# Kernel optimization log

Measured on AMD Instinct MI355X. Metric: run time of the kernel, lower is better.

Reference implementation:

```python
import jax, jax.numpy as jnp
import numpy as np

B, V, E = 8, 12288, 98304   # batch, nodes (healpix nside=32), edges (~8 nbrs/node)
FIN, FOUT, K = 256, 256, 4  # channels, Chebyshev order
EPS = 1e-5                  # BatchNorm1d eps


def setup_inputs() -> dict:
    key = jax.random.key(0)
    ks = jax.random.split(key, 5)
    x = jax.random.normal(ks[0], (B, V, FIN), jnp.float32)
    edge_src = jax.random.randint(ks[1], (E,), 0, V, dtype=jnp.int32)
    edge_dst = jax.random.randint(ks[2], (E,), 0, V, dtype=jnp.int32)
    edge_weight = jax.random.normal(ks[3], (E,), jnp.float32) * 0.3
    scale = (2.0 / (FIN * K)) ** 0.5  # kaiming-style init over K*Fin fan-in
    weight = jax.random.normal(ks[4], (K, FIN, FOUT), jnp.float32) * scale
    bias = jnp.zeros((FOUT,), jnp.float32)
    gamma = jnp.ones((FOUT,), jnp.float32)
    beta = jnp.zeros((FOUT,), jnp.float32)
    return {"x": x, "edge_weight": edge_weight, "weight": weight, "bias": bias,
            "gamma": gamma, "beta": beta, "edge_src": edge_src, "edge_dst": edge_dst}


def reference(x, edge_weight, weight, bias, gamma, beta, edge_src, edge_dst):
    # --- ConvCheb: Chebyshev polynomial recursion over sparse Laplacian ---
    xt = x.transpose(1, 0, 2)  # [V, B, Fin] (node-major for segment scatter)

    def lmul(y):  # sparse L @ y, y: [V, B, Fin]
        msg = edge_weight[:, None, None] * y[edge_src]          # [E, B, Fin]
        return jax.ops.segment_sum(msg, edge_dst, num_segments=V)

    xs = [xt]                                  # T_0(L) x = x
    if K > 1:
        xs.append(lmul(xt))                    # T_1(L) x = L x
    for _ in range(2, K):
        xs.append(2.0 * lmul(xs[-1]) - xs[-2])  # T_k = 2 L T_{k-1} - T_{k-2}
    xk = jnp.stack(xs)                         # [K, V, B, Fin]

    out = jnp.einsum('kvbi,kio->bvo', xk, weight) + bias  # [B, V, Fout]

    # --- BatchNorm1d over channels (training-mode batch stats over B,V) ---
    mean = out.mean(axis=(0, 1))
    var = out.var(axis=(0, 1))  # biased variance, as torch uses for normalization
    out = gamma * (out - mean) * jax.lax.rsqrt(var + EPS) + beta

    return jax.nn.relu(out)
```

## Files before the change

kernel.cpp:

```cpp
#include <hip/hip_runtime.h>

#define Vn    12288
#define En    98304
#define Mrows 98304

typedef unsigned short u16;
typedef u16   u16x8  __attribute__((ext_vector_type(8)));
typedef __bf16 bf16x8 __attribute__((ext_vector_type(8)));
typedef float f32x4  __attribute__((ext_vector_type(4)));

__device__ __forceinline__ float bf2f(u16 u) {
    union { float f; unsigned int i; } c; c.i = ((unsigned int)u) << 16; return c.f;
}
__device__ __forceinline__ u16 f2bf(float f) {
    union { float f; unsigned int i; } c; c.f = f;
    unsigned int r = c.i + 0x7fffu + ((c.i >> 16) & 1u);
    return (u16)(r >> 16);
}
__device__ __forceinline__ void load_lds16(const void* g, void* l) {
    __builtin_amdgcn_global_load_lds(
        (const __attribute__((address_space(1))) void*)g,
        (__attribute__((address_space(3))) void*)l, 16, 0, 0);
}

__global__ void cvt_k(const float* __restrict__ x, u16* __restrict__ xb) {
    int v = blockIdx.x;
    int t = threadIdx.x;
    int b = t >> 5, i = (t & 31) * 8;
    const float* p = x + ((size_t)b * Vn + v) * 256 + i;
    f32x4 a0 = *(const f32x4*)p;
    f32x4 a1 = *(const f32x4*)(p + 4);
    u16x8 r;
    #pragma unroll
    for (int j = 0; j < 4; ++j) { r[j] = f2bf(a0[j]); r[4 + j] = f2bf(a1[j]); }
    *(u16x8*)(xb + (size_t)v * 2048 + b * 256 + i) = r;
}

__global__ void wtrans_k(const float* __restrict__ w, u16* __restrict__ wt) {
    int kk = blockIdx.x;
    int o  = threadIdx.x;
    wt[(size_t)o * 1024 + kk] = f2bf(w[(size_t)kk * 256 + o]);
}

__global__ void count_k(const int* __restrict__ dst, int* __restrict__ counts) {
    int e = blockIdx.x * 256 + threadIdx.x;
    atomicAdd(&counts[dst[e]], 1);
}

__global__ void scan_k(const int* __restrict__ counts, int* __restrict__ row_start,
                       int* __restrict__ cursor) {
    __shared__ int par[1024];
    int t = threadIdx.x;
    int base = t * 12;
    int s = 0;
    #pragma unroll
    for (int i = 0; i < 12; ++i) s += counts[base + i];
    par[t] = s;
    __syncthreads();
    for (int off = 1; off < 1024; off <<= 1) {
        int v_ = (t >= off) ? par[t - off] : 0;
        __syncthreads();
        par[t] += v_;
        __syncthreads();
    }
    int run = (t == 0) ? 0 : par[t - 1];
    for (int i = 0; i < 12; ++i) {
        row_start[base + i] = run;
        cursor[base + i]    = run;
        run += counts[base + i];
    }
    if (t == 1023) row_start[Vn] = En;
}

__global__ void fill_k(const int* __restrict__ src, const int* __restrict__ dst,
                       const float* __restrict__ ew, int* __restrict__ cursor,
                       int* __restrict__ csr_src, float* __restrict__ csr_w) {
    int e = blockIdx.x * 256 + threadIdx.x;
    int d = dst[e];
    int p = atomicAdd(&cursor[d], 1);
    csr_src[p] = src[e];
    csr_w[p]   = ew[e];
}

template<int PREV>
__global__ __launch_bounds__(256)
void lmul_k(const u16* __restrict__ yb, const u16* __restrict__ prevb,
            u16* __restrict__ outb, const int* __restrict__ row_start,
            const int* __restrict__ csr_src, const float* __restrict__ csr_w)
{
    __shared__ int   s_s[256];
    __shared__ float s_w[256];
    int slice = blockIdx.x & 7;
    int v0    = (blockIdx.x >> 3) * 8;
    int tid   = threadIdx.x;
    int s0    = row_start[v0];
    int tot   = row_start[v0 + 8] - s0;
    if (tid < tot && tid < 256) {
        s_s[tid] = csr_src[s0 + tid];
        s_w[tid] = csr_w[s0 + tid];
    }
    __syncthreads();
    int g = tid >> 5, t = tid & 31;
    int v = v0 + g;
    int base = row_start[v] - s0;
    int cnt  = row_start[v + 1] - row_start[v];
    size_t soff = (size_t)slice * 256 + (size_t)t * 8;
    float acc[8] = {0.f,0.f,0.f,0.f,0.f,0.f,0.f,0.f};
    for (int j = 0; j < cnt; ++j) {
        int s; float w;
        if (base + j < 256) { s = s_s[base + j]; w = s_w[base + j]; }
        else { s = csr_src[s0 + base + j]; w = csr_w[s0 + base + j]; }
        u16x8 u = *(const u16x8*)(yb + (size_t)s * 2048 + soff);
        #pragma unroll
        for (int j8 = 0; j8 < 8; ++j8) acc[j8] += w * bf2f(u[j8]);
    }
    u16x8 r;
    if (PREV) {
        u16x8 pu = *(const u16x8*)(prevb + (size_t)v * 2048 + soff);
        #pragma unroll
        for (int j8 = 0; j8 < 8; ++j8) r[j8] = f2bf(2.0f * acc[j8] - bf2f(pu[j8]));
    } else {
        #pragma unroll
        for (int j8 = 0; j8 < 8; ++j8) r[j8] = f2bf(acc[j8]);
    }
    *(u16x8*)(outb + (size_t)v * 2048 + soff) = r;
}

__global__ __launch_bounds__(256)
void gemm_k(const u16* __restrict__ x0, const u16* __restrict__ x1,
            const u16* __restrict__ x2, const u16* __restrict__ x3,
            const u16* __restrict__ wt, const float* __restrict__ bias,
            float* __restrict__ outp, float* __restrict__ sums, float* __restrict__ sumsq)
{
    alignas(16) __shared__ char lds[40960];
    int tid  = threadIdx.x;
    int wave = tid >> 6;
    int lane = tid & 63;
    int m0   = blockIdx.x * 64;

    f32x4 acc[4][4];
    #pragma unroll
    for (int a = 0; a < 4; ++a)
        #pragma unroll
        for (int b = 0; b < 4; ++b) acc[a][b] = (f32x4){0.f,0.f,0.f,0.f};

    for (int kt = 0; kt < 16; ++kt) {
        int ks = kt >> 2;
        int k0 = (kt & 3) * 64;
        const u16* Ak = (ks == 0) ? x0 : (ks == 1) ? x1 : (ks == 2) ? x2 : x3;
        #pragma unroll
        for (int r = 0; r < 2; ++r) {
            int g  = (r * 4 + wave) * 64 + lane;
            int ml = g >> 3;
            int c  = (g & 7) ^ (ml & 7);
            load_lds16(Ak + ((size_t)(m0 + ml)) * 256 + k0 + c * 8,
                       lds + (r * 4 + wave) * 1024);
        }
        #pragma unroll
        for (int r = 0; r < 8; ++r) {
            int g = (r * 4 + wave) * 64 + lane;
            int o = g >> 3;
            int c = (g & 7) ^ (o & 7);
            load_lds16(wt + (size_t)o * 1024 + kt * 64 + c * 8,
                       lds + 8192 + (r * 4 + wave) * 1024);
        }
        __syncthreads();
        #pragma unroll
        for (int kstep = 0; kstep < 2; ++kstep) {
            int cidx = kstep * 4 + (lane >> 4);
            int row  = lane & 15;
            bf16x8 af[4], bfr[4];
            #pragma unroll
            for (int mt = 0; mt < 4; ++mt) {
                int m16 = mt * 16 + row;
                af[mt] = *(const bf16x8*)(lds + (size_t)(m16 * 8 + (cidx ^ (m16 & 7))) * 16);
            }
            #pragma unroll
            for (int nt = 0; nt < 4; ++nt) {
                int o = wave * 64 + nt * 16 + row;
                bfr[nt] = *(const bf16x8*)(lds + 8192 + (size_t)(o * 8 + (cidx ^ (o & 7))) * 16);
            }
            #pragma unroll
            for (int mt = 0; mt < 4; ++mt)
                #pragma unroll
                for (int nt = 0; nt < 4; ++nt)
                    acc[mt][nt] = __builtin_amdgcn_mfma_f32_16x16x32_bf16(
                        af[mt], bfr[nt], acc[mt][nt], 0, 0, 0);
        }
        __syncthreads();
    }
    int crow = lane & 15, quad = lane >> 4;
    #pragma unroll
    for (int nt = 0; nt < 4; ++nt) {
        int o = wave * 64 + nt * 16 + crow;
        float bv = bias[o];
        float ps = 0.f, pq = 0.f;
        #pragma unroll
        for (int mt = 0; mt < 4; ++mt) {
            #pragma unroll
            for (int r = 0; r < 4; ++r) {
                int m = m0 + mt * 16 + quad * 4 + r;
                float val = acc[mt][nt][r] + bv;
                outp[((size_t)((m & 7) * Vn + (m >> 3))) * 256 + o] = val;
                ps += val; pq += val * val;
            }
        }
        ps += __shfl_down(ps, 32, 64);  pq += __shfl_down(pq, 32, 64);
        ps += __shfl_down(ps, 16, 64);  pq += __shfl_down(pq, 16, 64);
        if (quad == 0) { atomicAdd(&sums[o], ps); atomicAdd(&sumsq[o], pq); }
    }
}

__global__ void finalize_k(const float* __restrict__ sums, const float* __restrict__ sumsq,
                           const float* __restrict__ gamma, const float* __restrict__ beta,
                           float* __restrict__ scale, float* __restrict__ shift) {
    int o = threadIdx.x;
    const float invM = 1.0f / (float)Mrows;
    float mean = sums[o] * invM;
    float var  = sumsq[o] * invM - mean * mean;
    float sc   = gamma[o] * rsqrtf(var + 1e-5f);
    scale[o] = sc;
    shift[o] = beta[o] - mean * sc;
}

__global__ void bn_relu_k(float* __restrict__ outp, const float* __restrict__ scale,
                          const float* __restrict__ shift) {
    __shared__ float ssc[256], ssh[256];
    int t = threadIdx.x;
    ssc[t] = scale[t]; ssh[t] = shift[t];
    __syncthreads();
    size_t idx = ((size_t)blockIdx.x * 256 + t) * 8;
    int o0 = (int)(idx & 255);
    f32x4 a = *(const f32x4*)(outp + idx);
    f32x4 c = *(const f32x4*)(outp + idx + 4);
    #pragma unroll
    for (int i = 0; i < 4; ++i) {
        a[i] = fmaxf(a[i] * ssc[o0 + i]     + ssh[o0 + i],     0.f);
        c[i] = fmaxf(c[i] * ssc[o0 + 4 + i] + ssh[o0 + 4 + i], 0.f);
    }
    *(f32x4*)(outp + idx)     = a;
    *(f32x4*)(outp + idx + 4) = c;
}

extern "C" void kernel_launch(void* const* d_in, const int* in_sizes, int n_in,
                              void* d_out, int out_size, void* d_ws, size_t ws_size,
                              hipStream_t stream) {
    const float* x     = (const float*)d_in[0];
    const float* ew    = (const float*)d_in[1];
    const float* w     = (const float*)d_in[2];
    const float* bias  = (const float*)d_in[3];
    const float* gamma = (const float*)d_in[4];
    const float* beta  = (const float*)d_in[5];
    const int*   esrc  = (const int*)d_in[6];
    const int*   edst  = (const int*)d_in[7];
    float* outp = (float*)d_out;
    char*  ws   = (char*)d_ws;

    u16*   xb        = (u16*)  (ws + 0);
    u16*   x1        = (u16*)  (ws + 50331648);
    u16*   x2        = (u16*)  (ws + 100663296);
    u16*   x3        = (u16*)  (ws + 150994944);
    u16*   wt        = (u16*)  (ws + 201326592);
    int*   csr_src   = (int*)  (ws + 201850880);
    float* csr_w     = (float*)(ws + 202244096);
    int*   counts    = (int*)  (ws + 202637312);
    int*   row_start = (int*)  (ws + 202686464);
    int*   cursor    = (int*)  (ws + 202735872);
    float* sums      = (float*)(ws + 202785024);
    float* sumsq     = (float*)(ws + 202786048);
    float* scale     = (float*)(ws + 202787072);
    float* shift     = (float*)(ws + 202788096);

    hipMemsetAsync(counts, 0, 49152, stream);
    hipMemsetAsync(sums, 0, 2048, stream);

    cvt_k<<<Vn, 256, 0, stream>>>(x, xb);
    wtrans_k<<<1024, 256, 0, stream>>>(w, wt);
    count_k<<<384, 256, 0, stream>>>(edst, counts);
    scan_k<<<1, 1024, 0, stream>>>(counts, row_start, cursor);
    fill_k<<<384, 256, 0, stream>>>(esrc, edst, ew, cursor, csr_src, csr_w);

    lmul_k<0><<<Vn, 256, 0, stream>>>(xb, nullptr, x1, row_start, csr_src, csr_w);
    lmul_k<1><<<Vn, 256, 0, stream>>>(x1, xb,      x2, row_start, csr_src, csr_w);
    lmul_k<1><<<Vn, 256, 0, stream>>>(x2, x1,      x3, row_start, csr_src, csr_w);

    gemm_k<<<Mrows / 64, 256, 0, stream>>>(xb, x1, x2, x3, wt, bias, outp, sums, sumsq);

    finalize_k<<<1, 256, 0, stream>>>(sums, sumsq, gamma, beta, scale, shift);
    bn_relu_k<<<12288, 256, 0, stream>>>(outp, scale, shift);
}
```

Measured before the change: 483.6 us.

## Pack CSR edges, unroll gather by four, and retile GEMM to 128x128

Edge source index and weight are stored together as one 8-byte struct. The sparse multiply now drops its LDS staging and barrier and issues four independent neighbor gathers per iteration to expose more memory-level parallelism. The GEMM switches from 64xfull-N tiles to 128x128 tiles, with 2x2 waves and two N halves per row band, which changes A/B reuse and the grid size. The A tile is now loaded twice across the two N halves, in exchange for less LDS per block and a different occupancy balance.

New measurement: 498.2 us. 1.03x slower.

```diff
diff --git a/kernel.cpp b/kernel.cpp
--- a/kernel.cpp
+++ b/kernel.cpp
@@ -8,6 +8,8 @@
 typedef u16   u16x8  __attribute__((ext_vector_type(8)));
 typedef __bf16 bf16x8 __attribute__((ext_vector_type(8)));
 typedef float f32x4  __attribute__((ext_vector_type(4)));
+
+struct __align__(8) Edge { int s; float w; };
 
 __device__ __forceinline__ float bf2f(u16 u) {
     union { float f; unsigned int i; } c; c.i = ((unsigned int)u) << 16; return c.f;
@@ -74,45 +76,44 @@
 
 __global__ void fill_k(const int* __restrict__ src, const int* __restrict__ dst,
                        const float* __restrict__ ew, int* __restrict__ cursor,
-                       int* __restrict__ csr_src, float* __restrict__ csr_w) {
+                       Edge* __restrict__ csr) {
     int e = blockIdx.x * 256 + threadIdx.x;
     int d = dst[e];
     int p = atomicAdd(&cursor[d], 1);
-    csr_src[p] = src[e];
-    csr_w[p]   = ew[e];
+    Edge ed; ed.s = src[e]; ed.w = ew[e];
+    csr[p] = ed;
 }
 
 template<int PREV>
 __global__ __launch_bounds__(256)
 void lmul_k(const u16* __restrict__ yb, const u16* __restrict__ prevb,
             u16* __restrict__ outb, const int* __restrict__ row_start,
-            const int* __restrict__ csr_src, const float* __restrict__ csr_w)
+            const Edge* __restrict__ csr)
 {
-    __shared__ int   s_s[256];
-    __shared__ float s_w[256];
     int slice = blockIdx.x & 7;
-    int v0    = (blockIdx.x >> 3) * 8;
-    int tid   = threadIdx.x;
-    int s0    = row_start[v0];
-    int tot   = row_start[v0 + 8] - s0;
-    if (tid < tot && tid < 256) {
-        s_s[tid] = csr_src[s0 + tid];
-        s_w[tid] = csr_w[s0 + tid];
-    }
-    __syncthreads();
-    int g = tid >> 5, t = tid & 31;
-    int v = v0 + g;
-    int base = row_start[v] - s0;
-    int cnt  = row_start[v + 1] - row_start[v];
+    int v     = (blockIdx.x >> 3) * 8 + (threadIdx.x >> 5);
+    int t     = threadIdx.x & 31;
+    int s0    = row_start[v];
+    int cnt   = row_start[v + 1] - s0;
     size_t soff = (size_t)slice * 256 + (size_t)t * 8;
     float acc[8] = {0.f,0.f,0.f,0.f,0.f,0.f,0.f,0.f};
-    for (int j = 0; j < cnt; ++j) {
-        int s; float w;
-        if (base + j < 256) { s = s_s[base + j]; w = s_w[base + j]; }
-        else { s = csr_src[s0 + base + j]; w = csr_w[s0 + base + j]; }
-        u16x8 u = *(const u16x8*)(yb + (size_t)s * 2048 + soff);
-        #pragma unroll
-        for (int j8 = 0; j8 < 8; ++j8) acc[j8] += w * bf2f(u[j8]);
+    for (int j0 = 0; j0 < cnt; j0 += 4) {
+        int ss[4]; float ww[4];
+        #pragma unroll
+        for (int u = 0; u < 4; ++u) {
+            int j = j0 + u;
+            bool ok = j < cnt;
+            Edge e = csr[s0 + (ok ? j : 0)];
+            ss[u] = e.s; ww[u] = ok ? e.w : 0.f;
+        }
+        u16x8 g[4];
+        #pragma unroll
+        for (int u = 0; u < 4; ++u)
+            g[u] = *(const u16x8*)(yb + (size_t)ss[u] * 2048 + soff);
+        #pragma unroll
+        for (int u = 0; u < 4; ++u)
+            #pragma unroll
+            for (int j8 = 0; j8 < 8; ++j8) acc[j8] += ww[u] * bf2f(g[u][j8]);
     }
     u16x8 r;
     if (PREV) {
@@ -132,11 +133,16 @@
             const u16* __restrict__ wt, const float* __restrict__ bias,
             float* __restrict__ outp, float* __restrict__ sums, float* __restrict__ sumsq)
 {
-    alignas(16) __shared__ char lds[40960];
+    alignas(16) __shared__ char lds[32768];
     int tid  = threadIdx.x;
     int wave = tid >> 6;
     int lane = tid & 63;
-    int m0   = blockIdx.x * 64;
+    int band = blockIdx.x % 768;
+    int half = blockIdx.x / 768;
+    int m0   = band * 128;
+    int n0   = half * 128;
+    int wm   = wave & 1;
+    int wn   = wave >> 1;
 
     f32x4 acc[4][4];
     #pragma unroll
@@ -149,7 +155,7 @@
         int k0 = (kt & 3) * 64;
         const u16* Ak = (ks == 0) ? x0 : (ks == 1) ? x1 : (ks == 2) ? x2 : x3;
         #pragma unroll
-        for (int r = 0; r < 2; ++r) {
+        for (int r = 0; r < 4; ++r) {
             int g  = (r * 4 + wave) * 64 + lane;
             int ml = g >> 3;
             int c  = (g & 7) ^ (ml & 7);
@@ -157,12 +163,12 @@
                        lds + (r * 4 + wave) * 1024);
         }
         #pragma unroll
-        for (int r = 0; r < 8; ++r) {
+        for (int r = 0; r < 4; ++r) {
             int g = (r * 4 + wave) * 64 + lane;
             int o = g >> 3;
             int c = (g & 7) ^ (o & 7);
-            load_lds16(wt + (size_t)o * 1024 + kt * 64 + c * 8,
-                       lds + 8192 + (r * 4 + wave) * 1024);
+            load_lds16(wt + (size_t)(n0 + o) * 1024 + kt * 64 + c * 8,
+                       lds + 16384 + (r * 4 + wave) * 1024);
         }
         __syncthreads();
         #pragma unroll
@@ -172,13 +178,13 @@
             bf16x8 af[4], bfr[4];
             #pragma unroll
             for (int mt = 0; mt < 4; ++mt) {
-                int m16 = mt * 16 + row;
+                int m16 = wm * 64 + mt * 16 + row;
                 af[mt] = *(const bf16x8*)(lds + (size_t)(m16 * 8 + (cidx ^ (m16 & 7))) * 16);
             }
             #pragma unroll
             for (int nt = 0; nt < 4; ++nt) {
-                int o = wave * 64 + nt * 16 + row;
-                bfr[nt] = *(const bf16x8*)(lds + 8192 + (size_t)(o * 8 + (cidx ^ (o & 7))) * 16);
+                int ol = wn * 64 + nt * 16 + row;
+                bfr[nt] = *(const bf16x8*)(lds + 16384 + (size_t)(ol * 8 + (cidx ^ (ol & 7))) * 16);
             }
             #pragma unroll
             for (int mt = 0; mt < 4; ++mt)
@@ -192,14 +198,14 @@
     int crow = lane & 15, quad = lane >> 4;
     #pragma unroll
     for (int nt = 0; nt < 4; ++nt) {
-        int o = wave * 64 + nt * 16 + crow;
+        int o = n0 + wn * 64 + nt * 16 + crow;
         float bv = bias[o];
         float ps = 0.f, pq = 0.f;
         #pragma unroll
         for (int mt = 0; mt < 4; ++mt) {
             #pragma unroll
             for (int r = 0; r < 4; ++r) {
-                int m = m0 + mt * 16 + quad * 4 + r;
+                int m = m0 + wm * 64 + mt * 16 + quad * 4 + r;
                 float val = acc[mt][nt][r] + bv;
                 outp[((size_t)((m & 7) * Vn + (m >> 3))) * 256 + o] = val;
                 ps += val; pq += val * val;
@@ -261,15 +267,14 @@
     u16*   x2        = (u16*)  (ws + 100663296);
     u16*   x3        = (u16*)  (ws + 150994944);
     u16*   wt        = (u16*)  (ws + 201326592);
-    int*   csr_src   = (int*)  (ws + 201850880);
-    float* csr_w     = (float*)(ws + 202244096);
+    Edge*  csr       = (Edge*) (ws + 201850880);
     int*   counts    = (int*)  (ws + 202637312);
     int*   row_start = (int*)  (ws + 202686464);
-    int*   cursor    = (int*)  (ws + 202735872);
-    float* sums      = (float*)(ws + 202785024);
-    float* sumsq     = (float*)(ws + 202786048);
-    float* scale     = (float*)(ws + 202787072);
-    float* shift     = (float*)(ws + 202788096);
+    int*   cursor    = (int*)  (ws + 202736128);
+    float* sums      = (float*)(ws + 202785280);
+    float* sumsq     = (float*)(ws + 202786304);
+    float* scale     = (float*)(ws + 202787328);
+    float* shift     = (float*)(ws + 202788352);
 
     hipMemsetAsync(counts, 0, 49152, stream);
     hipMemsetAsync(sums, 0, 2048, stream);
@@ -278,13 +283,13 @@
     wtrans_k<<<1024, 256, 0, stream>>>(w, wt);
     count_k<<<384, 256, 0, stream>>>(edst, counts);
     scan_k<<<1, 1024, 0, stream>>>(counts, row_start, cursor);
-    fill_k<<<384, 256, 0, stream>>>(esrc, edst, ew, cursor, csr_src, csr_w);
-
-    lmul_k<0><<<Vn, 256, 0, stream>>>(xb, nullptr, x1, row_start, csr_src, csr_w);
-    lmul_k<1><<<Vn, 256, 0, stream>>>(x1, xb,      x2, row_start, csr_src, csr_w);
-    lmul_k<1><<<Vn, 256, 0, stream>>>(x2, x1,      x3, row_start, csr_src, csr_w);
-
-    gemm_k<<<Mrows / 64, 256, 0, stream>>>(xb, x1, x2, x3, wt, bias, outp, sums, sumsq);
+    fill_k<<<384, 256, 0, stream>>>(esrc, edst, ew, cursor, csr);
+
+    lmul_k<0><<<Vn, 256, 0, stream>>>(xb, nullptr, x1, row_start, csr);
+    lmul_k<1><<<Vn, 256, 0, stream>>>(x1, xb,      x2, row_start, csr);
+    lmul_k<1><<<Vn, 256, 0, stream>>>(x2, x1,      x3, row_start, csr);
+
+    gemm_k<<<1536, 256, 0, stream>>>(xb, x1, x2, x3, wt, bias, outp, sums, sumsq);
 
     finalize_k<<<1, 256, 0, stream>>>(sums, sumsq, gamma, beta, scale, shift);
     bn_relu_k<<<12288, 256, 0, stream>>>(outp, scale, shift);
```
